# Kernel optimization log

Hardware: AMD Instinct MI355X
Metric: run time of the kernel (lower is better)

Reference implementation:

```python
import jax, jax.numpy as jnp
import numpy as np
import math

HID = 1152
NH = 16
HD = HID // NH            # 72
P = 2
DEPTH = 4
MLP_M = int(2.0 / 3.0 * int(HID * 4.0))  # 3072 (SwiGLU inner)
FREQ = 256
NCLS = 1000
ROPE_THETA = 10000.0


def rms_norm(x, w, eps=1e-6):
    return x * jax.lax.rsqrt(jnp.mean(jnp.square(x), axis=-1, keepdims=True) + eps) * w


def rotate_half(x):
    # interleaved pairs (a, b) -> (-b, a)
    x2 = x.reshape(x.shape[:-1] + (x.shape[-1] // 2, 2))
    a, b = x2[..., 0], x2[..., 1]
    return jnp.stack((-b, a), axis=-1).reshape(x.shape)


def make_rope(S, head_dim, theta=ROPE_THETA):
    # VisionRotaryEmbedder: per-axis rope dim = head_dim//2, 2 spatial axes concat
    d = head_dim // 2
    f = 1.0 / theta ** (jnp.arange(0, d, 2)[: d // 2].astype(jnp.float32) / d)
    fr = jnp.arange(S, dtype=jnp.float32)[:, None] * f[None, :]   # [S, d//2]
    fr = jnp.repeat(fr, 2, axis=-1)                               # [S, d]
    grid = jnp.concatenate(
        [jnp.broadcast_to(fr[:, None, :], (S, S, d)),
         jnp.broadcast_to(fr[None, :, :], (S, S, d))], axis=-1)   # [S, S, head_dim]
    grid = grid.reshape(S * S, head_dim)
    return jnp.cos(grid), jnp.sin(grid)


def timestep_embedding(t, dim=FREQ, max_period=10000.0):
    half = dim // 2
    freqs = jnp.exp(-math.log(max_period) * jnp.arange(half, dtype=jnp.float32) / half)
    args = t[:, None].astype(jnp.float32) * freqs[None, :]
    return jnp.concatenate([jnp.cos(args), jnp.sin(args)], axis=-1)


def setup_inputs() -> dict:
    key = jax.random.key(0)
    ks = jax.random.split(key, 24)
    s = 0.02
    B, C, H, W = 2, 4, 64, 64
    d = {
        'x': jax.random.normal(ks[0], (B, C, H, W), jnp.float32),
        't': jax.random.uniform(ks[1], (B,), jnp.float32),
        'y': jax.random.randint(ks[2], (B,), 0, NCLS),
        'patch_w': jax.random.normal(ks[3], (P * P * C, HID), jnp.float32) * s,
        'patch_b': jnp.zeros((HID,), jnp.float32),
        't_w1': jax.random.normal(ks[4], (FREQ, HID), jnp.float32) * s,
        't_b1': jnp.zeros((HID,), jnp.float32),
        't_w2': jax.random.normal(ks[5], (HID, HID), jnp.float32) * s,
        't_b2': jnp.zeros((HID,), jnp.float32),
        'y_table': jax.random.normal(ks[6], (NCLS + 1, HID), jnp.float32) * s,
        'norm1_w': jnp.ones((DEPTH, HID), jnp.float32),
        'qkv_w': jax.random.normal(ks[7], (DEPTH, HID, 3 * HID), jnp.float32) * s,
        'qkv_b': jnp.zeros((DEPTH, 3 * HID), jnp.float32),
        'out_w': jax.random.normal(ks[8], (DEPTH, HID, HID), jnp.float32) * s,
        'out_b': jnp.zeros((DEPTH, HID), jnp.float32),
        'norm2_w': jnp.ones((DEPTH, HID), jnp.float32),
        'mlp_w12': jax.random.normal(ks[9], (DEPTH, HID, 2 * MLP_M), jnp.float32) * s,
        'mlp_b12': jnp.zeros((DEPTH, 2 * MLP_M), jnp.float32),
        'mlp_w3': jax.random.normal(ks[10], (DEPTH, MLP_M, HID), jnp.float32) * s,
        'mlp_b3': jnp.zeros((DEPTH, HID), jnp.float32),
        'adaln_w': jax.random.normal(ks[11], (DEPTH, HID, 4 * HID), jnp.float32) * s,
        'adaln_b': jnp.zeros((DEPTH, 4 * HID), jnp.float32),
        'fnorm_w': jnp.ones((HID,), jnp.float32),
        'fadaln_w': jax.random.normal(ks[12], (HID, 2 * HID), jnp.float32) * s,
        'fadaln_b': jnp.zeros((2 * HID,), jnp.float32),
        'flin_w': jax.random.normal(ks[13], (HID, P * P * C), jnp.float32) * s,
        'flin_b': jnp.zeros((P * P * C,), jnp.float32),
    }
    return d


def reference(x, t, y, patch_w, patch_b, t_w1, t_b1, t_w2, t_b2, y_table,
              norm1_w, qkv_w, qkv_b, out_w, out_b, norm2_w,
              mlp_w12, mlp_b12, mlp_w3, mlp_b3, adaln_w, adaln_b,
              fnorm_w, fadaln_w, fadaln_b, flin_w, flin_b):
    B, C, H, W = x.shape
    S = H // P
    L = S * S
    # patchify -> [B, L, P*P*C] -> linear embed
    tok = x.reshape(B, C, S, P, S, P).transpose(0, 2, 4, 3, 5, 1).reshape(B, L, P * P * C)
    h = tok @ patch_w + patch_b
    # conditioning: timestep MLP + class embedding
    temb = timestep_embedding(t)
    temb = jax.nn.silu(temb @ t_w1 + t_b1) @ t_w2 + t_b2
    c = temb + y_table[y]
    c_silu = jax.nn.silu(c)
    cos, sin = make_rope(S, HD)  # [L, HD]
    scale = 1.0 / math.sqrt(HD)

    def block(hx, p):
        n1w, qw, qb, ow, ob, n2w, w12, b12, w3, b3, aw, ab = p
        mod = c_silu @ aw + ab  # [B, 4*HID]
        s_msa, g_msa, s_mlp, g_mlp = jnp.split(mod, 4, axis=-1)
        hmod = rms_norm(hx, n1w) * (1.0 + s_msa[:, None, :])
        qkv = (hmod @ qw + qb).reshape(B, L, 3, NH, HD)
        qkv = jnp.swapaxes(qkv, 1, 3)  # [B, NH, 3, L, HD]
        q, k, v = qkv[:, :, 0], qkv[:, :, 1], qkv[:, :, 2]
        q = q * cos + rotate_half(q) * sin
        k = k * cos + rotate_half(k) * sin
        w = jax.nn.softmax(jnp.einsum('bhqd,bhkd->bhqk', q, k) * scale, axis=-1)
        o = jnp.einsum('bhqk,bhkd->bhqd', w, v)
        o = jnp.swapaxes(o, 1, 2).reshape(B, L, HID) @ ow + ob
        hx = hx + g_msa[:, None, :] * o
        hmod2 = rms_norm(hx, n2w) * (1.0 + s_mlp[:, None, :])
        x12 = hmod2 @ w12 + b12
        x1, x2 = jnp.split(x12, 2, axis=-1)
        m = (jax.nn.silu(x1) * x2) @ w3 + b3
        hx = hx + g_mlp[:, None, :] * m
        return hx, None

    h, _ = jax.lax.scan(block, h, (norm1_w, qkv_w, qkv_b, out_w, out_b, norm2_w,
                                   mlp_w12, mlp_b12, mlp_w3, mlp_b3, adaln_w, adaln_b))

    # final layer: shift+scale modulation then zero-init linear (random here)
    fmod = c_silu @ fadaln_w + fadaln_b
    shift, fscale = jnp.split(fmod, 2, axis=-1)
    hf = rms_norm(h, fnorm_w) * (1.0 + fscale[:, None, :]) + shift[:, None, :]
    out = hf @ flin_w + flin_b  # [B, L, P*P*C]
    out = out.reshape(B, S, S, P, P, C).transpose(0, 5, 1, 3, 2, 4).reshape(B, C, H, W)
    return out
```

## Files before the change

kernel.cpp:

```cpp
#include <hip/hip_runtime.h>
#include <hip/hip_bf16.h>

#define HIDN 1152
#define NHEAD 16
#define HDIM 72
#define LTOK 1024
#define MTOK 2048
#define MLPM 3072

typedef short bf16x8 __attribute__((ext_vector_type(8)));
typedef float f32x4 __attribute__((ext_vector_type(4)));

__device__ __forceinline__ void gload16(const void* g, void* l) {
    __builtin_amdgcn_global_load_lds(
        (const __attribute__((address_space(1))) void*)g,
        (__attribute__((address_space(3))) void*)l,
        16, 0, 0);
}

__device__ __forceinline__ short bfbits(float f) {
    __hip_bfloat16 h = __float2bfloat16(f);
    return *(short*)&h;
}
__device__ __forceinline__ float bff(short s) {
    return __bfloat162float(*(__hip_bfloat16*)&s);
}

__device__ __forceinline__ void xcd_swizzle(int& bx, int& by) {
    int gx = gridDim.x;
    int wgid = blockIdx.y * gx + blockIdx.x;
    int cpx = (gx * gridDim.y) >> 3;
    int nid = (wgid & 7) * cpx + (wgid >> 3);
    bx = nid % gx;
    by = nid / gx;
}

__global__ __launch_bounds__(256) void k_patch(const float* __restrict__ x,
        const float* __restrict__ pw, const float* __restrict__ pb,
        __hip_bfloat16* __restrict__ h) {
    int m = blockIdx.x;
    int b = m >> 10, l = m & 1023;
    int si = l >> 5, sj = l & 31;
    __shared__ float toks[16];
    int tid = threadIdx.x;
    if (tid < 16) {
        int pi = tid >> 3, pj = (tid >> 2) & 1, c = tid & 3;
        toks[tid] = x[((size_t)(b*4 + c)*64 + si*2 + pi)*64 + sj*2 + pj];
    }
    __syncthreads();
    for (int o = tid; o < HIDN; o += 256) {
        float acc = pb[o];
        #pragma unroll
        for (int kk = 0; kk < 16; ++kk) acc += toks[kk] * pw[kk*HIDN + o];
        h[(size_t)m*HIDN + o] = __float2bfloat16(acc);
    }
}

__global__ __launch_bounds__(256) void k_temb1_v2(const float* __restrict__ t,
        const float* __restrict__ w1, const float* __restrict__ b1,
        float* __restrict__ temb1) {
    int jt = blockIdx.x, b = blockIdx.y;
    int tid = threadIdx.x;
    __shared__ float emb[256];
    __shared__ float red[128];
    float tv = t[b];
    if (tid < 128) { float f = __expf(-logf(10000.f) * (float)tid / 128.f);        emb[tid] = cosf(tv * f); }
    else           { float f = __expf(-logf(10000.f) * (float)(tid - 128) / 128.f); emb[tid] = sinf(tv * f); }
    __syncthreads();
    int o = jt*128 + (tid & 127), s = tid >> 7;
    float acc = 0.f;
    for (int k = s*128; k < s*128 + 128; ++k) acc += emb[k] * w1[(size_t)k*HIDN + o];
    if (s) red[tid & 127] = acc;
    __syncthreads();
    if (!s) {
        float v = acc + red[tid] + b1[o];
        temb1[b*HIDN + o] = v / (1.f + __expf(-v));
    }
}

__global__ __launch_bounds__(256) void k_csilu_s1(const float* __restrict__ temb1,
        const float* __restrict__ w2, float* __restrict__ csilup) {
    int jt = blockIdx.x, kz = blockIdx.y;
    int tid = threadIdx.x;
    __shared__ float t1s[2][288];
    __shared__ float red[2][128];
    for (int i = tid; i < 576; i += 256)
        t1s[i/288][i%288] = temb1[(i/288)*HIDN + kz*288 + (i%288)];
    __syncthreads();
    int o = jt*128 + (tid & 127), s = tid >> 7;
    float a0 = 0.f, a1 = 0.f;
    for (int i = s*144; i < s*144 + 144; ++i) {
        float wv = w2[(size_t)(kz*288 + i)*HIDN + o];
        a0 += t1s[0][i]*wv; a1 += t1s[1][i]*wv;
    }
    if (s) { red[0][tid & 127] = a0; red[1][tid & 127] = a1; }
    __syncthreads();
    if (!s) {
        csilup[(kz*2 + 0)*HIDN + o] = a0 + red[0][tid];
        csilup[(kz*2 + 1)*HIDN + o] = a1 + red[1][tid];
    }
}

__global__ __launch_bounds__(128) void k_csilu_s2(const float* __restrict__ csilup,
        const float* __restrict__ b2, const float* __restrict__ ytab,
        const int* __restrict__ y, float* __restrict__ csilu) {
    int o = blockIdx.x*128 + threadIdx.x;
    int b = blockIdx.y;
    float acc = b2[o] + ytab[(size_t)y[b]*HIDN + o];
    #pragma unroll
    for (int kz = 0; kz < 4; ++kz) acc += csilup[(kz*2 + b)*HIDN + o];
    csilu[b*HIDN + o] = acc / (1.f + __expf(-acc));
}

__global__ __launch_bounds__(256) void k_cond_s1(const float* __restrict__ csilu,
        const float* __restrict__ adaln_w, const float* __restrict__ fadaln_w,
        float* __restrict__ condp) {
    int ct = blockIdx.x, kz = blockIdx.y;
    int tid = threadIdx.x;
    int c0 = ct*128;
    const float* Wb; int rstride;
    if (c0 < 18432) { int d = c0/4608; Wb = adaln_w + (size_t)d*HIDN*4608 + (c0 % 4608); rstride = 4608; }
    else            { Wb = fadaln_w + (c0 - 18432); rstride = 2304; }
    __shared__ float cs[2][288];
    __shared__ float red[2][128];
    for (int i = tid; i < 576; i += 256)
        cs[i/288][i%288] = csilu[(i/288)*HIDN + kz*288 + (i%288)];
    __syncthreads();
    int o = tid & 127, s = tid >> 7;
    float a0 = 0.f, a1 = 0.f;
    for (int i = s*144; i < s*144 + 144; ++i) {
        float wv = Wb[(size_t)(kz*288 + i)*rstride + o];
        a0 += cs[0][i]*wv; a1 += cs[1][i]*wv;
    }
    if (s) { red[0][o] = a0; red[1][o] = a1; }
    __syncthreads();
    if (!s) {
        condp[((size_t)kz*2 + 0)*20736 + c0 + o] = a0 + red[0][o];
        condp[((size_t)kz*2 + 1)*20736 + c0 + o] = a1 + red[1][o];
    }
}

__global__ __launch_bounds__(256) void k_cond_s2(const float* __restrict__ condp,
        const float* __restrict__ adaln_b, const float* __restrict__ fadaln_b,
        float* __restrict__ modb, float* __restrict__ fmod) {
    int c = blockIdx.x*256 + threadIdx.x;
    int b = blockIdx.y;
    float acc = 0.f;
    #pragma unroll
    for (int kz = 0; kz < 4; ++kz) acc += condp[((size_t)kz*2 + b)*20736 + c];
    if (c < 18432) {
        int d = c/4608, j = c%4608;
        modb[((size_t)d*2 + b)*4608 + j] = acc + adaln_b[(size_t)d*4608 + j];
    } else {
        int j = c - 18432;
        fmod[(size_t)b*2304 + j] = acc + fadaln_b[j];
    }
}

__global__ __launch_bounds__(256) void k_rope(float* __restrict__ cosb, float* __restrict__ sinb) {
    int idx = blockIdx.x*256 + threadIdx.x;
    if (idx >= LTOK*HDIM) return;
    int l = idx / HDIM, dd = idx % HDIM;
    int i = l >> 5, j = l & 31;
    int pos = (dd < 36) ? i : j;
    int mm = ((dd < 36) ? dd : dd - 36) >> 1;
    float f = __expf(-logf(10000.f) * (float)mm / 18.f);
    float fr = (float)pos * f;
    cosb[idx] = cosf(fr);
    sinb[idx] = sinf(fr);
}

__global__ __launch_bounds__(256) void k_rms(const __hip_bfloat16* __restrict__ hx,
        const float* __restrict__ nw, const float* __restrict__ smod,
        __hip_bfloat16* __restrict__ outp) {
    int m = blockIdx.x; int b = m >> 10;
    int tid = threadIdx.x;
    const bf16x8* row8 = (const bf16x8*)(hx + (size_t)m*HIDN);
    bool act = tid < 144;
    float vals[8];
    float part = 0.f;
    if (act) {
        bf16x8 v = row8[tid];
        #pragma unroll
        for (int i = 0; i < 8; ++i) { float f = bff(v[i]); vals[i] = f; part += f*f; }
    }
    for (int off = 32; off; off >>= 1) part += __shfl_xor(part, off);
    __shared__ float wsum[4];
    if ((tid & 63) == 0) wsum[tid >> 6] = part;
    __syncthreads();
    float rs = rsqrtf((wsum[0]+wsum[1]+wsum[2]+wsum[3]) * (1.f/HIDN) + 1e-6f);
    if (act) {
        const float* nwp = nw + tid*8;
        const float* sbp = smod + (size_t)b*4608 + tid*8;
        bf16x8 o;
        #pragma unroll
        for (int i = 0; i < 8; ++i)
            o[i] = bfbits(vals[i] * rs * nwp[i] * (1.f + sbp[i]));
        *(bf16x8*)(outp + (size_t)m*HIDN + tid*8) = o;
    }
}

__global__ __launch_bounds__(256) void k_castT_all(
        const float* __restrict__ qkv_w, const float* __restrict__ out_w,
        const float* __restrict__ m12_w, const float* __restrict__ m3_w,
        __hip_bfloat16* __restrict__ wtb) {
    __shared__ float tile[128][65];
    int bid = blockIdx.x;
    int layer = bid / 1944, r = bid % 1944;
    const float* W; __hip_bfloat16* Wt; int K, N, nt, t; bool glu = false;
    __hip_bfloat16* bl = wtb + (size_t)layer*15925248;
    if (r < 486)       { t = r;        nt = 54; K = 1152; N = 3456; W = qkv_w + (size_t)layer*K*N; Wt = bl; }
    else if (r < 648)  { t = r - 486;  nt = 18; K = 1152; N = 1152; W = out_w + (size_t)layer*K*N; Wt = bl + 3981312; }
    else if (r < 1512) { t = r - 648;  nt = 96; K = 1152; N = 6144; W = m12_w + (size_t)layer*K*N; Wt = bl + 5308416; glu = true; }
    else               { t = r - 1512; nt = 18; K = 3072; N = 1152; W = m3_w  + (size_t)layer*K*N; Wt = bl + 12386304; }
    int n0 = (t % nt)*64, k0 = (t / nt)*128;
    int tid = threadIdx.x;
    int rr = tid >> 4, c4 = (tid & 15)*4;
    #pragma unroll
    for (int p = 0; p < 8; ++p) {
        int kk = p*16 + rr;
        float4 v = *(const float4*)(W + (size_t)(k0+kk)*N + n0 + c4);
        tile[kk][c4+0] = v.x; tile[kk][c4+1] = v.y; tile[kk][c4+2] = v.z; tile[kk][c4+3] = v.w;
    }
    __syncthreads();
    int seg = tid & 15, nn0 = tid >> 4;
    #pragma unroll
    for (int p = 0; p < 4; ++p) {
        int nn = p*16 + nn0;
        bf16x8 o;
        #pragma unroll
        for (int j = 0; j < 8; ++j) o[j] = bfbits(tile[seg*8 + j][nn]);
        int ng = n0 + nn;
        int np = glu ? ((ng < 3072) ? 2*ng : 2*(ng - 3072) + 1) : ng;
        *(bf16x8*)(Wt + (size_t)np*K + k0 + seg*8) = o;
    }
}

template<int EPI, typename OutT>
__global__ __launch_bounds__(256) void k_gemm_bf16(
        const __hip_bfloat16* __restrict__ A,
        const __hip_bfloat16* __restrict__ Wt,
        const float* __restrict__ bias,
        OutT* __restrict__ C, int M, int N, int K,
        const float* __restrict__ gate) {
    __shared__ __hip_bfloat16 Asm[2][128*64];
    __shared__ __hip_bfloat16 Bsm[2][128*64];
    int bx, by; xcd_swizzle(bx, by);
    int tid = threadIdx.x;
    int lane = tid & 63, w = tid >> 6;
    int wr = w >> 1, wc = w & 1;
    int m0 = by * 128, n0 = bx * 128;
    f32x4 acc[4][4] = {};
    int lr = lane >> 3, ls = lane & 7;
    int swz = ls ^ (lr & 7);
    int x7 = lane & 7;
    const __hip_bfloat16* Ag = A  + (size_t)(m0 + lr)*K + swz*8;
    const __hip_bfloat16* Bg = Wt + (size_t)(n0 + lr)*K + swz*8;
    int nk = K >> 6;
    #pragma unroll
    for (int i = 0; i < 4; ++i) {
        int seg = w*4 + i;
        gload16(Ag + (size_t)(seg*8)*K, (char*)&Asm[0][0] + seg*1024);
        gload16(Bg + (size_t)(seg*8)*K, (char*)&Bsm[0][0] + seg*1024);
    }
    __syncthreads();
    for (int t = 0; t < nk; ++t) {
        int cur = t & 1;
        if (t + 1 < nk) {
            int k1 = (t + 1) << 6;
            #pragma unroll
            for (int i = 0; i < 4; ++i) {
                int seg = w*4 + i;
                gload16(Ag + (size_t)(seg*8)*K + k1, (char*)&Asm[cur^1][0] + seg*1024);
                gload16(Bg + (size_t)(seg*8)*K + k1, (char*)&Bsm[cur^1][0] + seg*1024);
            }
        }
        const __hip_bfloat16* Ac = Asm[cur];
        const __hip_bfloat16* Bc = Bsm[cur];
        __builtin_amdgcn_s_setprio(1);
        #pragma unroll
        for (int kk = 0; kk < 2; ++kk) {
            bf16x8 af[4], bfr[4];
            #pragma unroll
            for (int m = 0; m < 4; ++m) {
                int row = wr*64 + m*16 + (lane&15);
                af[m] = *(const bf16x8*)(Ac + row*64 + (((kk*4 + (lane>>4)) ^ x7) * 8));
            }
            #pragma unroll
            for (int n = 0; n < 4; ++n) {
                int col = wc*64 + n*16 + (lane&15);
                bfr[n] = *(const bf16x8*)(Bc + col*64 + (((kk*4 + (lane>>4)) ^ x7) * 8));
            }
            #pragma unroll
            for (int m = 0; m < 4; ++m)
                #pragma unroll
                for (int n = 0; n < 4; ++n)
                    acc[m][n] = __builtin_amdgcn_mfma_f32_16x16x32_bf16(af[m], bfr[n], acc[m][n], 0, 0, 0);
        }
        __builtin_amdgcn_s_setprio(0);
        __syncthreads();
    }
    int r0 = (lane >> 4) * 4;
    int ccol = lane & 15;
    #pragma unroll
    for (int m = 0; m < 4; ++m) {
        #pragma unroll
        for (int rr = 0; rr < 4; ++rr) {
            int row = m0 + wr*64 + m*16 + r0 + rr;
            #pragma unroll
            for (int n = 0; n < 4; ++n) {
                int col = n0 + wc*64 + n*16 + ccol;
                if (EPI == 0) {
                    float val = acc[m][n][rr] + bias[col];
                    C[(size_t)row*N + col] = (OutT)__float2bfloat16(val);
                } else {
                    float val = acc[m][n][rr] + bias[(col & 1) ? 3072 + (col >> 1) : (col >> 1)];
                    float other = __shfl_xor(val, 1);
                    if (!(lane & 1)) {
                        float res = val / (1.f + __expf(-val)) * other;
                        ((__hip_bfloat16*)C)[(size_t)row*(N>>1) + (col>>1)] = __float2bfloat16(res);
                    }
                }
            }
        }
    }
}

__global__ __launch_bounds__(256) void k_gemm_qkv(
        const __hip_bfloat16* __restrict__ A,
        const __hip_bfloat16* __restrict__ Wt,
        const float* __restrict__ bias,
        const float* __restrict__ cosb, const float* __restrict__ sinb,
        __hip_bfloat16* __restrict__ q, __hip_bfloat16* __restrict__ k,
        __hip_bfloat16* __restrict__ v) {
    const int N = 3456, K = HIDN;
    __shared__ __hip_bfloat16 Asm[2][128*64];
    __shared__ __hip_bfloat16 Bsm[2][128*64];
    int bx, by; xcd_swizzle(bx, by);
    int tid = threadIdx.x;
    int lane = tid & 63, w = tid >> 6;
    int wr = w >> 1, wc = w & 1;
    int m0 = by * 128, n0 = bx * 128;
    f32x4 acc[4][4] = {};
    int lr = lane >> 3, ls = lane & 7;
    int swz = ls ^ (lr & 7);
    int x7 = lane & 7;
    const __hip_bfloat16* Ag = A  + (size_t)(m0 + lr)*K + swz*8;
    const __hip_bfloat16* Bg = Wt + (size_t)(n0 + lr)*K + swz*8;
    const int nk = K >> 6;
    #pragma unroll
    for (int i = 0; i < 4; ++i) {
        int seg = w*4 + i;
        gload16(Ag + (size_t)(seg*8)*K, (char*)&Asm[0][0] + seg*1024);
        gload16(Bg + (size_t)(seg*8)*K, (char*)&Bsm[0][0] + seg*1024);
    }
    __syncthreads();
    for (int t = 0; t < nk; ++t) {
        int cur = t & 1;
        if (t + 1 < nk) {
            int k1 = (t + 1) << 6;
            #pragma unroll
            for (int i = 0; i < 4; ++i) {
                int seg = w*4 + i;
                gload16(Ag + (size_t)(seg*8)*K + k1, (char*)&Asm[cur^1][0] + seg*1024);
                gload16(Bg + (size_t)(seg*8)*K + k1, (char*)&Bsm[cur^1][0] + seg*1024);
            }
        }
        const __hip_bfloat16* Ac = Asm[cur];
        const __hip_bfloat16* Bc = Bsm[cur];
        __builtin_amdgcn_s_setprio(1);
        #pragma unroll
        for (int kk = 0; kk < 2; ++kk) {
            bf16x8 af[4], bfr[4];
            #pragma unroll
            for (int m = 0; m < 4; ++m) {
                int row = wr*64 + m*16 + (lane&15);
                af[m] = *(const bf16x8*)(Ac + row*64 + (((kk*4 + (lane>>4)) ^ x7) * 8));
            }
            #pragma unroll
            for (int n = 0; n < 4; ++n) {
                int col = wc*64 + n*16 + (lane&15);
                bfr[n] = *(const bf16x8*)(Bc + col*64 + (((kk*4 + (lane>>4)) ^ x7) * 8));
            }
            #pragma unroll
            for (int m = 0; m < 4; ++m)
                #pragma unroll
                for (int n = 0; n < 4; ++n)
                    acc[m][n] = __builtin_amdgcn_mfma_f32_16x16x32_bf16(af[m], bfr[n], acc[m][n], 0, 0, 0);
        }
        __builtin_amdgcn_s_setprio(0);
        __syncthreads();
    }
    int r0 = (lane >> 4) * 4;
    int ccol = lane & 15;
    int sec = n0 / 1152;
    int rembase = n0 - sec*1152 + wc*64;
    #pragma unroll
    for (int m = 0; m < 4; ++m) {
        #pragma unroll
        for (int rr = 0; rr < 4; ++rr) {
            int row = m0 + wr*64 + m*16 + r0 + rr;
            int b = row >> 10, l = row & 1023;
            #pragma unroll
            for (int n = 0; n < 4; ++n) {
                int rem = rembase + n*16 + ccol;
                int h = rem / HDIM, d = rem % HDIM;
                float val = acc[m][n][rr] + bias[sec*1152 + rem];
                if (sec == 2) {
                    v[((size_t)(b*NHEAD + h)*HDIM + d)*LTOK + l] = __float2bfloat16(val);
                } else {
                    float c = cosb[l*HDIM + d], s = sinb[l*HDIM + d];
                    float other = __shfl_xor(val, 1);
                    float res = (d & 1) ? (val*c + other*s) : (val*c - other*s);
                    __hip_bfloat16 hv = __float2bfloat16(res);
                    size_t dst = ((size_t)(b*NHEAD + h)*LTOK + l)*HDIM + d;
                    if (sec == 0) q[dst] = hv; else k[dst] = hv;
                }
            }
        }
    }
}

__global__ __launch_bounds__(256) void k_gemm32(
        const __hip_bfloat16* __restrict__ A,
        const __hip_bfloat16* __restrict__ Wt,
        const float* __restrict__ bias,
        __hip_bfloat16* __restrict__ C, int M, int N, int K,
        const float* __restrict__ gate) {
    __shared__ __hip_bfloat16 Asm[2][32*64];
    __shared__ __hip_bfloat16 Bsm[2][128*64];
    int bx, by; xcd_swizzle(bx, by);
    int tid = threadIdx.x;
    int lane = tid & 63, w = tid >> 6;
    int wr = w >> 1, wc = w & 1;
    int m0 = by * 32, n0 = bx * 128;
    f32x4 acc[4] = {};
    int lr = lane >> 3, ls = lane & 7;
    int swz = ls ^ (lr & 7);
    int x7 = lane & 7;
    const __hip_bfloat16* Ag = A  + (size_t)(m0 + lr)*K + swz*8;
    const __hip_bfloat16* Bg = Wt + (size_t)(n0 + lr)*K + swz*8;
    int nk = K >> 6;
    gload16(Ag + (size_t)(w*8)*K, (char*)&Asm[0][0] + w*1024);
    #pragma unroll
    for (int i = 0; i < 4; ++i) {
        int seg = w*4 + i;
        gload16(Bg + (size_t)(seg*8)*K, (char*)&Bsm[0][0] + seg*1024);
    }
    __syncthreads();
    for (int t = 0; t < nk; ++t) {
        int cur = t & 1;
        if (t + 1 < nk) {
            int k1 = (t + 1) << 6;
            gload16(Ag + (size_t)(w*8)*K + k1, (char*)&Asm[cur^1][0] + w*1024);
            #pragma unroll
            for (int i = 0; i < 4; ++i) {
                int seg = w*4 + i;
                gload16(Bg + (size_t)(seg*8)*K + k1, (char*)&Bsm[cur^1][0] + seg*1024);
            }
        }
        const __hip_bfloat16* Ac = Asm[cur];
        const __hip_bfloat16* Bc = Bsm[cur];
        __builtin_amdgcn_s_setprio(1);
        #pragma unroll
        for (int kk = 0; kk < 2; ++kk) {
            int row = wr*16 + (lane&15);
            bf16x8 af = *(const bf16x8*)(Ac + row*64 + (((kk*4 + (lane>>4)) ^ x7) * 8));
            #pragma unroll
            for (int n = 0; n < 4; ++n) {
                int col = wc*64 + n*16 + (lane&15);
                bf16x8 bfr = *(const bf16x8*)(Bc + col*64 + (((kk*4 + (lane>>4)) ^ x7) * 8));
                acc[n] = __builtin_amdgcn_mfma_f32_16x16x32_bf16(af, bfr, acc[n], 0, 0, 0);
            }
        }
        __builtin_amdgcn_s_setprio(0);
        __syncthreads();
    }
    int r0 = (lane >> 4) * 4;
    int ccol = lane & 15;
    #pragma unroll
    for (int rr = 0; rr < 4; ++rr) {
        int row = m0 + wr*16 + r0 + rr;
        int bi = row >> 10;
        #pragma unroll
        for (int n = 0; n < 4; ++n) {
            int col = n0 + wc*64 + n*16 + ccol;
            float val = acc[n][rr] + bias[col];
            size_t idx = (size_t)row*N + col;
            float prev = __bfloat162float(C[idx]);
            C[idx] = __float2bfloat16(prev + gate[(size_t)bi*4608 + col] * val);
        }
    }
}

__global__ __launch_bounds__(512) void k_attn_mfma(
        const __hip_bfloat16* __restrict__ q,
        const __hip_bfloat16* __restrict__ k,
        const __hip_bfloat16* __restrict__ vt,
        __hip_bfloat16* __restrict__ o) {
    int x = blockIdx.x;
    int head_id = (x & 7)*4 + (x >> 6);
    int qt = (x >> 3) & 7;
    int b = head_id >> 4, h = head_id & 15;
    const float scale = 0.117851130f;
    __shared__ __hip_bfloat16 Ksm[2][64*72];
    __shared__ __hip_bfloat16 Vsm[2][72*64];
    __shared__ __hip_bfloat16 Psm[8][16*72];
    int tid = threadIdx.x, lane = tid & 63, w = tid >> 6;
    int l15 = lane & 15, g = lane >> 4;
    const __hip_bfloat16* qg = q  + ((size_t)(b*NHEAD + h)*LTOK + qt*128)*HDIM;
    const __hip_bfloat16* kg = k  + (size_t)(b*NHEAD + h)*LTOK*HDIM;
    const __hip_bfloat16* vg = vt + (size_t)(b*NHEAD + h)*HDIM*LTOK;
    const bf16x8 z = {};

    bf16x8 qf[3];
    {
        const __hip_bfloat16* qrow = qg + (w*16 + l15)*HDIM;
        qf[0] = *(const bf16x8*)(qrow + g*8);
        qf[1] = *(const bf16x8*)(qrow + 32 + g*8);
        qf[2] = (g == 0) ? *(const bf16x8*)(qrow + 64) : z;
    }
    int vsw  = ((lane & 7) ^ (lane >> 3)) * 8;
    int vrow = lane >> 3;

    f32x4 oacc[5] = {};
    float mold[4] = {-1e30f, -1e30f, -1e30f, -1e30f};
    float lsum[4] = {};

    {
        for (int s = w; s < 9; s += 8) {
            gload16(kg + s*512 + lane*8, (char*)&Ksm[0][0] + s*1024);
            gload16(vg + (size_t)(s*8 + vrow)*LTOK + vsw, (char*)&Vsm[0][0] + s*1024);
        }
    }
    __syncthreads();

    for (int kt2 = 0; kt2 < 16; ++kt2) {
        int cur = kt2 & 1;
        if (kt2 < 15) {
            const __hip_bfloat16* ktg = kg + (size_t)(kt2+1)*64*HDIM;
            const __hip_bfloat16* vtg = vg + (kt2+1)*64;
            for (int s = w; s < 9; s += 8) {
                gload16(ktg + s*512 + lane*8, (char*)&Ksm[cur^1][0] + s*1024);
                gload16(vtg + (size_t)(s*8 + vrow)*LTOK + vsw, (char*)&Vsm[cur^1][0] + s*1024);
            }
        }
        const __hip_bfloat16* Kc = Ksm[cur];
        const __hip_bfloat16* Vc = Vsm[cur];
        f32x4 st[4] = {};
        __builtin_amdgcn_s_setprio(1);
        #pragma unroll
        for (int t = 0; t < 4; ++t) {
            const __hip_bfloat16* krow = Kc + (t*16 + l15)*72;
            bf16x8 kf0 = *(const bf16x8*)(krow + g*8);
            bf16x8 kf1 = *(const bf16x8*)(krow + 32 + g*8);
            bf16x8 kf2 = (g == 0) ? *(const bf16x8*)(krow + 64) : z;
            st[t] = __builtin_amdgcn_mfma_f32_16x16x32_bf16(qf[0], kf0, st[t], 0, 0, 0);
            st[t] = __builtin_amdgcn_mfma_f32_16x16x32_bf16(qf[1], kf1, st[t], 0, 0, 0);
            st[t] = __builtin_amdgcn_mfma_f32_16x16x32_bf16(qf[2], kf2, st[t], 0, 0, 0);
        }
        __builtin_amdgcn_s_setprio(0);
        float mtr[4];
        #pragma unroll
        for (int r = 0; r < 4; ++r) {
            float mt = fmaxf(fmaxf(st[0][r], st[1][r]), fmaxf(st[2][r], st[3][r]));
            mt = fmaxf(mt, __shfl_xor(mt, 1));
            mt = fmaxf(mt, __shfl_xor(mt, 2));
            mt = fmaxf(mt, __shfl_xor(mt, 4));
            mt = fmaxf(mt, __shfl_xor(mt, 8));
            mtr[r] = mt;
        }
        bool need = false;
        #pragma unroll
        for (int r = 0; r < 4; ++r) need |= (mtr[r] - mold[r]) * scale > 8.f;
        if (__any(need)) {
            #pragma unroll
            for (int r = 0; r < 4; ++r) {
                float mn = fmaxf(mold[r], mtr[r]);
                float corr = __expf((mold[r] - mn) * scale);
                mold[r] = mn;
                lsum[r] *= corr;
                #pragma unroll
                for (int dt = 0; dt < 5; ++dt) oacc[dt][r] *= corr;
            }
        }
        #pragma unroll
        for (int r = 0; r < 4; ++r) {
            float rs = 0.f;
            #pragma unroll
            for (int t = 0; t < 4; ++t) {
                float p = __expf((st[t][r] - mold[r]) * scale);
                rs += p;
                Psm[w][(g*4 + r)*72 + t*16 + l15] = __float2bfloat16(p);
            }
            rs += __shfl_xor(rs, 1);
            rs += __shfl_xor(rs, 2);
            rs += __shfl_xor(rs, 4);
            rs += __shfl_xor(rs, 8);
            lsum[r] += rs;
        }
        bf16x8 pa0 = *(const bf16x8*)(&Psm[w][l15*72 + g*8]);
        bf16x8 pa1 = *(const bf16x8*)(&Psm[w][l15*72 + 32 + g*8]);
        int cswz = (l15 & 7)*8;
        __builtin_amdgcn_s_setprio(1);
        #pragma unroll
        for (int dt = 0; dt < 5; ++dt) {
            int row = dt*16 + l15;
            bool valid = (dt < 4) | (l15 < 8);
            bf16x8 vf0 = valid ? *(const bf16x8*)(Vc + row*64 + ((g*8) ^ cswz)) : z;
            bf16x8 vf1 = valid ? *(const bf16x8*)(Vc + row*64 + ((32 + g*8) ^ cswz)) : z;
            oacc[dt] = __builtin_amdgcn_mfma_f32_16x16x32_bf16(pa0, vf0, oacc[dt], 0, 0, 0);
            oacc[dt] = __builtin_amdgcn_mfma_f32_16x16x32_bf16(pa1, vf1, oacc[dt], 0, 0, 0);
        }
        __builtin_amdgcn_s_setprio(0);
        __syncthreads();
    }
    #pragma unroll
    for (int r = 0; r < 4; ++r) {
        float inv = 1.f / lsum[r];
        int row = qt*128 + w*16 + g*4 + r;
        __hip_bfloat16* op = o + ((size_t)b*LTOK + row)*HIDN + h*HDIM;
        #pragma unroll
        for (int dt = 0; dt < 5; ++dt) {
            int d = dt*16 + l15;
            if (d < HDIM) op[d] = __float2bfloat16(oacc[dt][r] * inv);
        }
    }
}

__global__ __launch_bounds__(256) void k_final(const __hip_bfloat16* __restrict__ hx,
        const float* __restrict__ fnw, const float* __restrict__ fmod,
        const float* __restrict__ flw, const float* __restrict__ flb,
        float* __restrict__ out) {
    int m = blockIdx.x; int b = m >> 10, l = m & 1023;
    int tid = threadIdx.x;
    const bf16x8* row8 = (const bf16x8*)(hx + (size_t)m*HIDN);
    bool act = tid < 144;
    float vals[8];
    float part = 0.f;
    if (act) {
        bf16x8 v = row8[tid];
        #pragma unroll
        for (int i = 0; i < 8; ++i) { float f = bff(v[i]); vals[i] = f; part += f*f; }
    }
    for (int off = 32; off; off >>= 1) part += __shfl_xor(part, off);
    __shared__ float wsum[4];
    __shared__ float hfs[HIDN];
    __shared__ float red[4][16];
    if ((tid & 63) == 0) wsum[tid >> 6] = part;
    __syncthreads();
    float rs = rsqrtf((wsum[0]+wsum[1]+wsum[2]+wsum[3]) * (1.f/HIDN) + 1e-6f);
    if (act) {
        const float* fm = fmod + (size_t)b*2304;
        #pragma unroll
        for (int i = 0; i < 8; ++i) {
            int j = tid*8 + i;
            hfs[j] = vals[i] * rs * fnw[j] * (1.f + fm[HIDN + j]) + fm[j];
        }
    }
    __syncthreads();
    float pacc[16] = {};
    for (int j = tid; j < HIDN; j += 256) {
        float hv = hfs[j];
        #pragma unroll
        for (int kk = 0; kk < 16; ++kk) pacc[kk] += hv * flw[j*16 + kk];
    }
    #pragma unroll
    for (int kk = 0; kk < 16; ++kk)
        for (int off = 32; off; off >>= 1) pacc[kk] += __shfl_xor(pacc[kk], off);
    if ((tid & 63) == 0) {
        int w = tid >> 6;
        #pragma unroll
        for (int kk = 0; kk < 16; ++kk) red[w][kk] = pacc[kk];
    }
    __syncthreads();
    if (tid < 16) {
        float val = red[0][tid] + red[1][tid] + red[2][tid] + red[3][tid] + flb[tid];
        int pi = tid >> 3, pj = (tid >> 2) & 1, c = tid & 3;
        int si = l >> 5, sj = l & 31;
        out[((size_t)(b*4 + c)*64 + si*2 + pi)*64 + sj*2 + pj] = val;
    }
}

extern "C" void kernel_launch(void* const* d_in, const int* in_sizes, int n_in,
                              void* d_out, int out_size, void* d_ws, size_t ws_size,
                              hipStream_t stream) {
    const float* x        = (const float*)d_in[0];
    const float* t        = (const float*)d_in[1];
    const int*   y        = (const int*)  d_in[2];
    const float* patch_w  = (const float*)d_in[3];
    const float* patch_b  = (const float*)d_in[4];
    const float* t_w1     = (const float*)d_in[5];
    const float* t_b1     = (const float*)d_in[6];
    const float* t_w2     = (const float*)d_in[7];
    const float* t_b2     = (const float*)d_in[8];
    const float* y_table  = (const float*)d_in[9];
    const float* norm1_w  = (const float*)d_in[10];
    const float* qkv_w    = (const float*)d_in[11];
    const float* qkv_b    = (const float*)d_in[12];
    const float* out_w    = (const float*)d_in[13];
    const float* out_b    = (const float*)d_in[14];
    const float* norm2_w  = (const float*)d_in[15];
    const float* mlp_w12  = (const float*)d_in[16];
    const float* mlp_b12  = (const float*)d_in[17];
    const float* mlp_w3   = (const float*)d_in[18];
    const float* mlp_b3   = (const float*)d_in[19];
    const float* adaln_w  = (const float*)d_in[20];
    const float* adaln_b  = (const float*)d_in[21];
    const float* fnorm_w  = (const float*)d_in[22];
    const float* fadaln_w = (const float*)d_in[23];
    const float* fadaln_b = (const float*)d_in[24];
    const float* flin_w   = (const float*)d_in[25];
    const float* flin_b   = (const float*)d_in[26];

    char* base = (char*)d_ws;
    __hip_bfloat16* hx    = (__hip_bfloat16*)(base);
    __hip_bfloat16* qbf   = (__hip_bfloat16*)(base + 34603008);
    __hip_bfloat16* kbf   = (__hip_bfloat16*)(base + 39321600);
    __hip_bfloat16* vbf   = (__hip_bfloat16*)(base + 44040192);
    __hip_bfloat16* hbf   = (__hip_bfloat16*)(base + 48758784);
    __hip_bfloat16* mhbf  = qbf;
    __hip_bfloat16* wtb   = (__hip_bfloat16*)(base + 53477376);
    float* temb1 = (float*)(base + 180879360);
    float* csilu = (float*)(base + 180888576);
    float* modb  = (float*)(base + 180897792);
    float* fmod  = (float*)(base + 181045248);
    float* cosb  = (float*)(base + 181063680);
    float* sinb  = (float*)(base + 181358592);
    float* condp = (float*)(base + 181653504);
    float* csilup= (float*)(base + 182317056);

    k_patch<<<2048, 256, 0, stream>>>(x, patch_w, patch_b, hx);
    k_temb1_v2<<<dim3(9,2), 256, 0, stream>>>(t, t_w1, t_b1, temb1);
    k_csilu_s1<<<dim3(9,4), 256, 0, stream>>>(temb1, t_w2, csilup);
    k_csilu_s2<<<dim3(9,2), 128, 0, stream>>>(csilup, t_b2, y_table, y, csilu);
    k_cond_s1<<<dim3(162,4), 256, 0, stream>>>(csilu, adaln_w, fadaln_w, condp);
    k_cond_s2<<<dim3(81,2), 256, 0, stream>>>(condp, adaln_b, fadaln_b, modb, fmod);
    k_rope<<<288, 256, 0, stream>>>(cosb, sinb);
    k_castT_all<<<7776, 256, 0, stream>>>(qkv_w, out_w, mlp_w12, mlp_w3, wtb);

    for (int d = 0; d < 4; ++d) {
        const float* modd = modb + (size_t)d*2*4608;
        __hip_bfloat16* wl = wtb + (size_t)d*15925248;
        __hip_bfloat16* wt_qkv = wl;
        __hip_bfloat16* wt_out = wl + 3981312;
        __hip_bfloat16* wt_m12 = wl + 5308416;
        __hip_bfloat16* wt_m3  = wl + 12386304;

        k_rms<<<2048, 256, 0, stream>>>(hx, norm1_w + d*HIDN, modd + 0*HIDN, hbf);
        k_gemm_qkv<<<dim3(27,16), 256, 0, stream>>>(hbf, wt_qkv, qkv_b + d*3456,
                cosb, sinb, qbf, kbf, vbf);
        k_attn_mfma<<<256, 512, 0, stream>>>(qbf, kbf, vbf, hbf);
        k_gemm32<<<dim3(9,64), 256, 0, stream>>>(hbf, wt_out,
                out_b + d*HIDN, hx, MTOK, HIDN, HIDN, modd + 1*HIDN);
        k_rms<<<2048, 256, 0, stream>>>(hx, norm2_w + d*HIDN, modd + 2*HIDN, hbf);
        k_gemm_bf16<2, __hip_bfloat16><<<dim3(48,16), 256, 0, stream>>>(hbf, wt_m12,
                mlp_b12 + d*6144, mhbf, MTOK, 6144, HIDN, nullptr);
        k_gemm32<<<dim3(9,64), 256, 0, stream>>>(mhbf, wt_m3,
                mlp_b3 + d*HIDN, hx, MTOK, HIDN, MLPM, modd + 3*HIDN);
    }
    k_final<<<2048, 256, 0, stream>>>(hx, fnorm_w, fmod, flin_w, flin_b, (float*)d_out);
}
```

Before: 978.9 us.

## Split attention into single-wave blocks reading K/V directly from global memory

The attention kernel changes from 512-thread blocks of 8 waves, which shared double-buffered K/V tiles in LDS, to 2048 single-wave blocks that each handle 16 query rows. Each wave now loads K and V fragments straight from global memory, with no LDS staging, no barriers and no setprio hints. The goal is to remove synchronisation and LDS overhead and to raise the number of independent waves. The cost is that K/V reuse across waves now depends on the cache, so global traffic per head goes up and the V loads are strided without the swizzle.

```diff
diff --git a/kernel.cpp b/kernel.cpp
--- a/kernel.cpp
+++ b/kernel.cpp
@@ -493,73 +493,56 @@
     }
 }
 
-__global__ __launch_bounds__(512) void k_attn_mfma(
+__global__ __launch_bounds__(64) void k_attn_mfma(
         const __hip_bfloat16* __restrict__ q,
         const __hip_bfloat16* __restrict__ k,
         const __hip_bfloat16* __restrict__ vt,
         __hip_bfloat16* __restrict__ o) {
     int x = blockIdx.x;
-    int head_id = (x & 7)*4 + (x >> 6);
-    int qt = (x >> 3) & 7;
+    int xcd = x & 7;
+    int within = x >> 3;
+    int head_local = within >> 6;
+    int qt = within & 63;
+    int head_id = xcd*4 + head_local;
     int b = head_id >> 4, h = head_id & 15;
     const float scale = 0.117851130f;
-    __shared__ __hip_bfloat16 Ksm[2][64*72];
-    __shared__ __hip_bfloat16 Vsm[2][72*64];
-    __shared__ __hip_bfloat16 Psm[8][16*72];
-    int tid = threadIdx.x, lane = tid & 63, w = tid >> 6;
+    __shared__ __hip_bfloat16 Psm[16*72];
+    int lane = threadIdx.x & 63;
     int l15 = lane & 15, g = lane >> 4;
-    const __hip_bfloat16* qg = q  + ((size_t)(b*NHEAD + h)*LTOK + qt*128)*HDIM;
+    const __hip_bfloat16* qg = q  + ((size_t)(b*NHEAD + h)*LTOK + qt*16)*HDIM;
     const __hip_bfloat16* kg = k  + (size_t)(b*NHEAD + h)*LTOK*HDIM;
     const __hip_bfloat16* vg = vt + (size_t)(b*NHEAD + h)*HDIM*LTOK;
     const bf16x8 z = {};
 
     bf16x8 qf[3];
     {
-        const __hip_bfloat16* qrow = qg + (w*16 + l15)*HDIM;
+        const __hip_bfloat16* qrow = qg + l15*HDIM;
         qf[0] = *(const bf16x8*)(qrow + g*8);
         qf[1] = *(const bf16x8*)(qrow + 32 + g*8);
         qf[2] = (g == 0) ? *(const bf16x8*)(qrow + 64) : z;
     }
-    int vsw  = ((lane & 7) ^ (lane >> 3)) * 8;
-    int vrow = lane >> 3;
 
     f32x4 oacc[5] = {};
     float mold[4] = {-1e30f, -1e30f, -1e30f, -1e30f};
     float lsum[4] = {};
 
-    {
-        for (int s = w; s < 9; s += 8) {
-            gload16(kg + s*512 + lane*8, (char*)&Ksm[0][0] + s*1024);
-            gload16(vg + (size_t)(s*8 + vrow)*LTOK + vsw, (char*)&Vsm[0][0] + s*1024);
-        }
-    }
-    __syncthreads();
-
-    for (int kt2 = 0; kt2 < 16; ++kt2) {
-        int cur = kt2 & 1;
-        if (kt2 < 15) {
-            const __hip_bfloat16* ktg = kg + (size_t)(kt2+1)*64*HDIM;
-            const __hip_bfloat16* vtg = vg + (kt2+1)*64;
-            for (int s = w; s < 9; s += 8) {
-                gload16(ktg + s*512 + lane*8, (char*)&Ksm[cur^1][0] + s*1024);
-                gload16(vtg + (size_t)(s*8 + vrow)*LTOK + vsw, (char*)&Vsm[cur^1][0] + s*1024);
-            }
-        }
-        const __hip_bfloat16* Kc = Ksm[cur];
-        const __hip_bfloat16* Vc = Vsm[cur];
+    for (int kt = 0; kt < 16; ++kt) {
+        const __hip_bfloat16* kb = kg + (size_t)kt*64*HDIM;
+        bf16x8 kf[4][3];
+        #pragma unroll
+        for (int t = 0; t < 4; ++t) {
+            const __hip_bfloat16* krow = kb + (t*16 + l15)*HDIM;
+            kf[t][0] = *(const bf16x8*)(krow + g*8);
+            kf[t][1] = *(const bf16x8*)(krow + 32 + g*8);
+            kf[t][2] = (g == 0) ? *(const bf16x8*)(krow + 64) : z;
+        }
         f32x4 st[4] = {};
-        __builtin_amdgcn_s_setprio(1);
         #pragma unroll
         for (int t = 0; t < 4; ++t) {
-            const __hip_bfloat16* krow = Kc + (t*16 + l15)*72;
-            bf16x8 kf0 = *(const bf16x8*)(krow + g*8);
-            bf16x8 kf1 = *(const bf16x8*)(krow + 32 + g*8);
-            bf16x8 kf2 = (g == 0) ? *(const bf16x8*)(krow + 64) : z;
-            st[t] = __builtin_amdgcn_mfma_f32_16x16x32_bf16(qf[0], kf0, st[t], 0, 0, 0);
-            st[t] = __builtin_amdgcn_mfma_f32_16x16x32_bf16(qf[1], kf1, st[t], 0, 0, 0);
-            st[t] = __builtin_amdgcn_mfma_f32_16x16x32_bf16(qf[2], kf2, st[t], 0, 0, 0);
-        }
-        __builtin_amdgcn_s_setprio(0);
+            st[t] = __builtin_amdgcn_mfma_f32_16x16x32_bf16(qf[0], kf[t][0], st[t], 0, 0, 0);
+            st[t] = __builtin_amdgcn_mfma_f32_16x16x32_bf16(qf[1], kf[t][1], st[t], 0, 0, 0);
+            st[t] = __builtin_amdgcn_mfma_f32_16x16x32_bf16(qf[2], kf[t][2], st[t], 0, 0, 0);
+        }
         float mtr[4];
         #pragma unroll
         for (int r = 0; r < 4; ++r) {
@@ -591,7 +574,7 @@
             for (int t = 0; t < 4; ++t) {
                 float p = __expf((st[t][r] - mold[r]) * scale);
                 rs += p;
-                Psm[w][(g*4 + r)*72 + t*16 + l15] = __float2bfloat16(p);
+                Psm[(g*4 + r)*72 + t*16 + l15] = __float2bfloat16(p);
             }
             rs += __shfl_xor(rs, 1);
             rs += __shfl_xor(rs, 2);
@@ -599,26 +582,23 @@
             rs += __shfl_xor(rs, 8);
             lsum[r] += rs;
         }
-        bf16x8 pa0 = *(const bf16x8*)(&Psm[w][l15*72 + g*8]);
-        bf16x8 pa1 = *(const bf16x8*)(&Psm[w][l15*72 + 32 + g*8]);
-        int cswz = (l15 & 7)*8;
-        __builtin_amdgcn_s_setprio(1);
+        bf16x8 pa0 = *(const bf16x8*)(&Psm[l15*72 + g*8]);
+        bf16x8 pa1 = *(const bf16x8*)(&Psm[l15*72 + 32 + g*8]);
         #pragma unroll
         for (int dt = 0; dt < 5; ++dt) {
             int row = dt*16 + l15;
             bool valid = (dt < 4) | (l15 < 8);
-            bf16x8 vf0 = valid ? *(const bf16x8*)(Vc + row*64 + ((g*8) ^ cswz)) : z;
-            bf16x8 vf1 = valid ? *(const bf16x8*)(Vc + row*64 + ((32 + g*8) ^ cswz)) : z;
+            const __hip_bfloat16* vrow = vg + (size_t)row*LTOK + kt*64;
+            bf16x8 vf0 = valid ? *(const bf16x8*)(vrow + g*8) : z;
+            bf16x8 vf1 = valid ? *(const bf16x8*)(vrow + 32 + g*8) : z;
             oacc[dt] = __builtin_amdgcn_mfma_f32_16x16x32_bf16(pa0, vf0, oacc[dt], 0, 0, 0);
             oacc[dt] = __builtin_amdgcn_mfma_f32_16x16x32_bf16(pa1, vf1, oacc[dt], 0, 0, 0);
         }
-        __builtin_amdgcn_s_setprio(0);
-        __syncthreads();
     }
     #pragma unroll
     for (int r = 0; r < 4; ++r) {
         float inv = 1.f / lsum[r];
-        int row = qt*128 + w*16 + g*4 + r;
+        int row = qt*16 + g*4 + r;
         __hip_bfloat16* op = o + ((size_t)b*LTOK + row)*HIDN + h*HDIM;
         #pragma unroll
         for (int dt = 0; dt < 5; ++dt) {
@@ -750,7 +730,7 @@
         k_rms<<<2048, 256, 0, stream>>>(hx, norm1_w + d*HIDN, modd + 0*HIDN, hbf);
         k_gemm_qkv<<<dim3(27,16), 256, 0, stream>>>(hbf, wt_qkv, qkv_b + d*3456,
                 cosb, sinb, qbf, kbf, vbf);
-        k_attn_mfma<<<256, 512, 0, stream>>>(qbf, kbf, vbf, hbf);
+        k_attn_mfma<<<2048, 64, 0, stream>>>(qbf, kbf, vbf, hbf);
         k_gemm32<<<dim3(9,64), 256, 0, stream>>>(hbf, wt_out,
                 out_b + d*HIDN, hx, MTOK, HIDN, HIDN, modd + 1*HIDN);
         k_rms<<<2048, 256, 0, stream>>>(hx, norm2_w + d*HIDN, modd + 2*HIDN, hbf);
```

New measurement: 1.051 ms. +7.3%, slower.
